# Performance work log

Measured on AMD Instinct MI355X. Metric: run time of the kernel, lower is better.

The kernel has to match this reference:

```python
import jax, jax.numpy as jnp
import numpy as np

NEG_SLOPE = 0.2   # PyG GATConv default leaky_relu slope
BN_EPS = 1e-5
SM_EPS = 1e-16    # PyG segment-softmax denominator epsilon


def gat_conv(x, src, dst, W, a_src, a_dst, bias, heads, out_ch, concat):
    # x: [N, F_in]; src/dst: [E] (self-loops already included)
    N = x.shape[0]
    h = (x @ W).reshape(N, heads, out_ch)              # [N, H, C]
    s = jnp.sum(h * a_src, axis=-1)                    # [N, H] per-node source score
    d = jnp.sum(h * a_dst, axis=-1)                    # [N, H] per-node dest score
    e = jax.nn.leaky_relu(s[src] + d[dst], NEG_SLOPE)  # [E, H]
    # segment softmax over edges grouped by destination node
    m = jax.ops.segment_max(e, dst, num_segments=N)
    m = jnp.where(jnp.isfinite(m), m, 0.0)
    p = jnp.exp(e - m[dst])                            # [E, H]
    denom = jax.ops.segment_sum(p, dst, num_segments=N)
    alpha = p / (denom[dst] + SM_EPS)                  # [E, H]
    # attention-weighted scatter-sum aggregation
    out = jax.ops.segment_sum(h[src] * alpha[:, :, None], dst, num_segments=N)  # [N, H, C]
    if concat:
        out = out.reshape(N, heads * out_ch)
    else:
        out = out.mean(axis=1)
    return out + bias


def setup_inputs() -> dict:
    key = jax.random.key(0)
    ks = jax.random.split(key, 12)
    N, E = 50000, 400000
    F_in, hidden, H1, H2, nclasses = 256, 64, 4, 1, 40
    x = jax.random.normal(ks[0], (N, F_in), dtype=jnp.float32)
    edge_index = jax.random.randint(ks[1], (2, E), 0, N, dtype=jnp.int64)
    g = 1.0 / np.sqrt(F_in)
    W1 = jax.random.normal(ks[2], (F_in, H1 * hidden), dtype=jnp.float32) * g
    a_src1 = jax.random.normal(ks[3], (H1, hidden), dtype=jnp.float32) * 0.1
    a_dst1 = jax.random.normal(ks[4], (H1, hidden), dtype=jnp.float32) * 0.1
    b1 = jnp.zeros((H1 * hidden,), dtype=jnp.float32)
    gamma = jnp.ones((H1 * hidden,), dtype=jnp.float32)
    beta = jnp.zeros((H1 * hidden,), dtype=jnp.float32)
    g2 = 1.0 / np.sqrt(H1 * hidden)
    W2 = jax.random.normal(ks[5], (H1 * hidden, H2 * nclasses), dtype=jnp.float32) * g2
    a_src2 = jax.random.normal(ks[6], (H2, nclasses), dtype=jnp.float32) * 0.1
    a_dst2 = jax.random.normal(ks[7], (H2, nclasses), dtype=jnp.float32) * 0.1
    b2 = jnp.zeros((nclasses,), dtype=jnp.float32)
    return {"x": x, "edge_index": edge_index, "W1": W1, "a_src1": a_src1,
            "a_dst1": a_dst1, "b1": b1, "gamma": gamma, "beta": beta,
            "W2": W2, "a_src2": a_src2, "a_dst2": a_dst2, "b2": b2}


def reference(x, edge_index, W1, a_src1, a_dst1, b1, gamma, beta, W2, a_src2, a_dst2, b2):
    N = x.shape[0]
    loop = jnp.arange(N, dtype=edge_index.dtype)
    src = jnp.concatenate([edge_index[0], loop])   # add self-loops (GATConv default)
    dst = jnp.concatenate([edge_index[1], loop])
    H1, hidden = a_src1.shape
    H2, nclasses = a_src2.shape
    h = gat_conv(x, src, dst, W1, a_src1, a_dst1, b1, H1, hidden, concat=True)
    # BatchNorm1d (training-mode batch statistics, biased variance)
    mu = h.mean(axis=0)
    var = h.var(axis=0)
    h = (h - mu) * jax.lax.rsqrt(var + BN_EPS) * gamma + beta
    h = jax.nn.elu(h)
    out = gat_conv(h, src, dst, W2, a_src2, a_dst2, b2, H2, nclasses, concat=False)
    return jax.nn.log_softmax(out, axis=-1)
```

## Files before the change

kernel.cpp:

```cpp
#include <hip/hip_runtime.h>
#include <hip/hip_fp16.h>

constexpr int FIN = 256;
constexpr int C1  = 256;
constexpr int HID = 64;
constexpr int H1N = 4;
constexpr int NC  = 40;
constexpr int CAP = 256;
constexpr int CAP2 = 128;

using f16x8 = __attribute__((ext_vector_type(8))) _Float16;
using f32x4 = __attribute__((ext_vector_type(4))) float;

__global__ __launch_bounds__(64)
void detect_kernel(const int* __restrict__ ei, int* __restrict__ flag, int E)
{
    int lane = threadIdx.x;
    int q = lane * (E / 64);
    int v = ei[2 * q + 1];
    unsigned long long nz = __ballot(v != 0);
    if (lane == 0) flag[0] = (nz == 0ull) ? 2 : 1;
}

__global__ __launch_bounds__(256)
void init_kernel(int* __restrict__ counts, int* __restrict__ fill,
                 float* __restrict__ colsum, float* __restrict__ colsq, int N)
{
    int t = blockIdx.x * 256 + threadIdx.x;
    if (t < N) { counts[t] = 1; fill[t] = 0; }
    if (t < C1) { colsum[t] = 0.f; colsq[t] = 0.f; }
}

__global__ __launch_bounds__(256)
void xcast_kernel(const float* __restrict__ X, _Float16* __restrict__ Xh,
                  int N, int NPAD)
{
    int idx = (blockIdx.x * 256 + threadIdx.x) * 4;
    if (idx >= NPAD * FIN) return;
    int row = idx >> 8;
    _Float16 h4[4];
    if (row < N) {
        float4 v = *(const float4*)(X + idx);
        h4[0] = (_Float16)v.x; h4[1] = (_Float16)v.y;
        h4[2] = (_Float16)v.z; h4[3] = (_Float16)v.w;
    } else {
        h4[0] = h4[1] = h4[2] = h4[3] = (_Float16)0.f;
    }
    *(uint2*)(Xh + idx) = *(uint2*)h4;
}

__global__ __launch_bounds__(256)
void w1cast_kernel(const float* __restrict__ W1, _Float16* __restrict__ W1t)
{
    __shared__ float tile[64][65];
    int bx = blockIdx.x & 3, by = blockIdx.x >> 2;
    int t = threadIdx.x;
    int c = t & 63, r4 = (t >> 6) * 16;
    #pragma unroll
    for (int i = 0; i < 16; ++i)
        tile[r4 + i][c] = W1[(size_t)(by * 64 + r4 + i) * C1 + bx * 64 + c];
    __syncthreads();
    #pragma unroll
    for (int i = 0; i < 16; ++i)
        W1t[(size_t)(bx * 64 + r4 + i) * FIN + by * 64 + c] =
            (_Float16)tile[c][r4 + i];
}

__global__ __launch_bounds__(256)
void gemm1_mfma_kernel(const _Float16* __restrict__ Xh,
                       const _Float16* __restrict__ W1t,
                       const float* __restrict__ as1, const float* __restrict__ ad1,
                       __half* __restrict__ Hm, float* __restrict__ s1,
                       float* __restrict__ d1, int N)
{
    const int t    = threadIdx.x;
    const int lane = t & 63;
    const int w    = t >> 6;
    const int rowbase = blockIdx.x * 64 + w * 16;
    const int lrow = lane & 15;
    const int kgrp = lane >> 4;
    const int arow = rowbase + lrow;

    f32x4 acc[16];
    #pragma unroll
    for (int i = 0; i < 16; ++i) acc[i] = f32x4{0.f, 0.f, 0.f, 0.f};

    #pragma unroll
    for (int ks = 0; ks < 8; ++ks) {
        f16x8 a = *(const f16x8*)(Xh + (size_t)arow * FIN + ks * 32 + kgrp * 8);
        #pragma unroll
        for (int ct = 0; ct < 16; ++ct) {
            f16x8 b = *(const f16x8*)(W1t + (size_t)(ct * 16 + lrow) * FIN
                                      + ks * 32 + kgrp * 8);
            acc[ct] = __builtin_amdgcn_mfma_f32_16x16x32_f16(a, b, acc[ct], 0, 0, 0);
        }
    }

    #pragma unroll
    for (int reg = 0; reg < 4; ++reg) {
        int r = rowbase + kgrp * 4 + reg;
        bool ok = r < N;
        #pragma unroll
        for (int h = 0; h < 4; ++h) {
            float sp = 0.f, dp = 0.f;
            #pragma unroll
            for (int q = 0; q < 4; ++q) {
                int ct = h * 4 + q;
                float v = acc[ct][reg];
                sp += v * as1[ct * 16 + lrow];
                dp += v * ad1[ct * 16 + lrow];
            }
            sp += __shfl_xor(sp, 1); sp += __shfl_xor(sp, 2);
            sp += __shfl_xor(sp, 4); sp += __shfl_xor(sp, 8);
            dp += __shfl_xor(dp, 1); dp += __shfl_xor(dp, 2);
            dp += __shfl_xor(dp, 4); dp += __shfl_xor(dp, 8);
            if (ok && lrow == 0) {
                s1[r * H1N + h] = sp;
                d1[r * H1N + h] = dp;
            }
        }
        if (ok) {
            #pragma unroll
            for (int ct = 0; ct < 16; ++ct)
                Hm[(size_t)r * C1 + ct * 16 + lrow] = __float2half(acc[ct][reg]);
        }
    }
}

__global__ __launch_bounds__(256)
void hist_kernel(const int* __restrict__ ei, const int* __restrict__ flag,
                 int* __restrict__ counts, int E)
{
    int t = blockIdx.x * 256 + threadIdx.x;
    int stride = flag[0];
    if (t < E) atomicAdd(&counts[ei[(size_t)stride * (E + t)]], 1);
}

__global__ __launch_bounds__(1024)
void scan_kernel(const int* __restrict__ cnt, int* __restrict__ offs, int N)
{
    __shared__ int wsum[16];
    __shared__ int carry_s;
    const int t = threadIdx.x, lane = t & 63, w = t >> 6;
    if (t == 0) carry_s = 0;
    __syncthreads();
    for (int base = 0; base < N; base += 1024) {
        int idx = base + t;
        int v = (idx < N) ? cnt[idx] : 0;
        int incl = v;
        #pragma unroll
        for (int off = 1; off < 64; off <<= 1) {
            int u = __shfl_up(incl, off);
            if (lane >= off) incl += u;
        }
        if (lane == 63) wsum[w] = incl;
        __syncthreads();
        int wpre = 0;
        for (int i = 0; i < w; ++i) wpre += wsum[i];
        int c = carry_s;
        if (idx < N) offs[idx] = c + wpre + incl - v;
        __syncthreads();
        if (t == 1023) carry_s = c + wpre + incl;
        __syncthreads();
    }
    if (t == 0) offs[N] = carry_s;
}

__global__ __launch_bounds__(256)
void scatter_kernel(const int* __restrict__ ei, const int* __restrict__ flag,
                    const int* __restrict__ offs, int* __restrict__ fill,
                    int* __restrict__ ssrc, int E, int N)
{
    int t = blockIdx.x * 256 + threadIdx.x;
    if (t >= E + N) return;
    int stride = flag[0];
    int s, d;
    if (t < E) {
        s = ei[(size_t)stride * t];
        d = ei[(size_t)stride * (E + t)];
    } else {
        s = t - E; d = s;
    }
    int pos = offs[d] + atomicAdd(&fill[d], 1);
    ssrc[pos] = s;
}

__global__ __launch_bounds__(256)
void agg1_kernel(const __half* __restrict__ Hm, const float* __restrict__ s1,
                 const float* __restrict__ d1, const int* __restrict__ offs,
                 const int* __restrict__ ssrc, const float* __restrict__ b1,
                 float* __restrict__ out1, int N)
{
    __shared__ float alpha[H1N][CAP];
    __shared__ int   srcs[CAP];
    __shared__ float invs[H1N];
    const int n    = blockIdx.x;
    const int t    = threadIdx.x;
    const int lane = t & 63;
    const int w    = t >> 6;
    const int beg  = offs[n], end = offs[n + 1];
    const int deg  = end - beg;
    const float dh = d1[n * H1N + w];

    if (deg <= CAP) {
        float mloc = -1e30f;
        for (int i = lane; i < deg; i += 64) {
            int s = ssrc[beg + i];
            if (w == 0) srcs[i] = s;
            float e = s1[s * H1N + w] + dh;
            e = e > 0.f ? e : 0.2f * e;
            alpha[w][i] = e;
            mloc = fmaxf(mloc, e);
        }
        #pragma unroll
        for (int off = 32; off; off >>= 1) mloc = fmaxf(mloc, __shfl_xor(mloc, off));
        float ssum = 0.f;
        for (int i = lane; i < deg; i += 64) {
            float ex = __expf(alpha[w][i] - mloc);
            alpha[w][i] = ex;
            ssum += ex;
        }
        #pragma unroll
        for (int off = 32; off; off >>= 1) ssum += __shfl_xor(ssum, off);
        if (lane == 0) invs[w] = 1.f / (ssum + 1e-16f);
        __syncthreads();

        float acc0 = 0.f, acc1 = 0.f, acc2 = 0.f, acc3 = 0.f;
        int i = 0;
        for (; i + 4 <= deg; i += 4) {
            int s0 = srcs[i],     s1i = srcs[i + 1];
            int s2 = srcs[i + 2], s3i = srcs[i + 3];
            float a0 = alpha[w][i],     a1 = alpha[w][i + 1];
            float a2 = alpha[w][i + 2], a3 = alpha[w][i + 3];
            float v0 = __half2float(Hm[(size_t)s0  * C1 + t]);
            float v1 = __half2float(Hm[(size_t)s1i * C1 + t]);
            float v2 = __half2float(Hm[(size_t)s2  * C1 + t]);
            float v3 = __half2float(Hm[(size_t)s3i * C1 + t]);
            acc0 += v0 * a0; acc1 += v1 * a1;
            acc2 += v2 * a2; acc3 += v3 * a3;
        }
        for (; i < deg; ++i)
            acc0 += __half2float(Hm[(size_t)srcs[i] * C1 + t]) * alpha[w][i];
        float acc = (acc0 + acc1) + (acc2 + acc3);
        out1[(size_t)n * C1 + t] = acc * invs[w] + b1[t];
        return;
    }

    float mloc = -1e30f;
    for (int p = beg + lane; p < end; p += 64) {
        float e = s1[ssrc[p] * H1N + w] + dh;
        e = e > 0.f ? e : 0.2f * e;
        mloc = fmaxf(mloc, e);
    }
    #pragma unroll
    for (int off = 32; off; off >>= 1) mloc = fmaxf(mloc, __shfl_xor(mloc, off));
    float ssum = 0.f;
    for (int p = beg + lane; p < end; p += 64) {
        float e = s1[ssrc[p] * H1N + w] + dh;
        e = e > 0.f ? e : 0.2f * e;
        ssum += __expf(e - mloc);
    }
    #pragma unroll
    for (int off = 32; off; off >>= 1) ssum += __shfl_xor(ssum, off);
    if (lane == 0) invs[w] = 1.f / (ssum + 1e-16f);

    float acc0 = 0.f, acc1 = 0.f, acc2 = 0.f, acc3 = 0.f;
    for (int c0 = 0; c0 < deg; c0 += CAP) {
        int cnt = min(CAP, deg - c0);
        for (int i = lane; i < cnt; i += 64) {
            int p = beg + c0 + i;
            int s = ssrc[p];
            if (w == 0) srcs[i] = s;
            float e = s1[s * H1N + w] + dh;
            e = e > 0.f ? e : 0.2f * e;
            alpha[w][i] = __expf(e - mloc);
        }
        __syncthreads();
        int i = 0;
        for (; i + 4 <= cnt; i += 4) {
            int s0 = srcs[i],     s1i = srcs[i + 1];
            int s2 = srcs[i + 2], s3i = srcs[i + 3];
            float a0 = alpha[w][i],     a1 = alpha[w][i + 1];
            float a2 = alpha[w][i + 2], a3 = alpha[w][i + 3];
            float v0 = __half2float(Hm[(size_t)s0  * C1 + t]);
            float v1 = __half2float(Hm[(size_t)s1i * C1 + t]);
            float v2 = __half2float(Hm[(size_t)s2  * C1 + t]);
            float v3 = __half2float(Hm[(size_t)s3i * C1 + t]);
            acc0 += v0 * a0; acc1 += v1 * a1;
            acc2 += v2 * a2; acc3 += v3 * a3;
        }
        for (; i < cnt; ++i)
            acc0 += __half2float(Hm[(size_t)srcs[i] * C1 + t]) * alpha[w][i];
        __syncthreads();
    }
    float acc = (acc0 + acc1) + (acc2 + acc3);
    out1[(size_t)n * C1 + t] = acc * invs[w] + b1[t];
}

__global__ __launch_bounds__(256)
void bnstats_kernel(const float* __restrict__ out1, float* __restrict__ colsum,
                    float* __restrict__ colsq, int N)
{
    int t = threadIdx.x;
    float s = 0.f, q = 0.f;
    for (int r = blockIdx.x; r < N; r += gridDim.x) {
        float v = out1[(size_t)r * C1 + t];
        s += v; q += v * v;
    }
    atomicAdd(&colsum[t], s);
    atomicAdd(&colsq[t], q);
}

__global__ __launch_bounds__(256)
void bnfin_kernel(const float* __restrict__ colsum, const float* __restrict__ colsq,
                  const float* __restrict__ gamma, const float* __restrict__ beta,
                  float* __restrict__ scale, float* __restrict__ shift, int N)
{
    int t = threadIdx.x;
    float mu  = colsum[t] / (float)N;
    float var = colsq[t] / (float)N - mu * mu;
    float sc  = gamma[t] * rsqrtf(var + 1e-5f);
    scale[t] = sc;
    shift[t] = beta[t] - mu * sc;
}

__global__ __launch_bounds__(256)
void gemm2_kernel(const float* __restrict__ out1, const float* __restrict__ scale,
                  const float* __restrict__ shift, const float* __restrict__ W2,
                  const float* __restrict__ as2, const float* __restrict__ ad2,
                  float* __restrict__ h2, float* __restrict__ s2,
                  float* __restrict__ d2, int N)
{
    __shared__ float Asm[64][68];
    __shared__ float Wsm[64 * 48];
    const int t   = threadIdx.x;
    const int r   = t >> 2;
    const int jg  = t & 3;
    const int rb  = blockIdx.x * 64;
    const int row = rb + r;
    const int j0  = jg * 10;

    float acc[10] = {};

    for (int kc = 0; kc < C1; kc += 64) {
        #pragma unroll
        for (int idx = t; idx < 64 * 16; idx += 256) {
            int ar = idx >> 4;
            int cg = (idx & 15) * 4;
            int arow = rb + ar;
            float4 v = make_float4(0.f, 0.f, 0.f, 0.f);
            if (arow < N) {
                v = *(const float4*)(out1 + (size_t)arow * C1 + kc + cg);
                float4 sc = *(const float4*)(scale + kc + cg);
                float4 sh = *(const float4*)(shift + kc + cg);
                v.x = v.x * sc.x + sh.x;
                v.y = v.y * sc.y + sh.y;
                v.z = v.z * sc.z + sh.z;
                v.w = v.w * sc.w + sh.w;
                v.x = v.x > 0.f ? v.x : (__expf(v.x) - 1.f);
                v.y = v.y > 0.f ? v.y : (__expf(v.y) - 1.f);
                v.z = v.z > 0.f ? v.z : (__expf(v.z) - 1.f);
                v.w = v.w > 0.f ? v.w : (__expf(v.w) - 1.f);
            }
            *(float4*)&Asm[ar][cg] = v;
        }
        #pragma unroll
        for (int idx = t; idx < 64 * 40; idx += 256) {
            int k = idx / 40, j = idx - k * 40;
            Wsm[k * 48 + (j / 10) * 12 + (j % 10)] = W2[(size_t)(kc + k) * NC + j];
        }
        __syncthreads();
        #pragma unroll 4
        for (int k = 0; k < 64; ++k) {
            float a = Asm[r][k];
            const float* wp = &Wsm[k * 48 + jg * 12];
            float4 w0 = *(const float4*)(wp);
            float4 w1 = *(const float4*)(wp + 4);
            float2 wv = *(const float2*)(wp + 8);
            acc[0] += a * w0.x; acc[1] += a * w0.y;
            acc[2] += a * w0.z; acc[3] += a * w0.w;
            acc[4] += a * w1.x; acc[5] += a * w1.y;
            acc[6] += a * w1.z; acc[7] += a * w1.w;
            acc[8] += a * wv.x; acc[9] += a * wv.y;
        }
        __syncthreads();
    }

    float sp = 0.f, dp = 0.f;
    #pragma unroll
    for (int jj = 0; jj < 10; ++jj) {
        sp += acc[jj] * as2[j0 + jj];
        dp += acc[jj] * ad2[j0 + jj];
    }
    sp += __shfl_xor(sp, 1); sp += __shfl_xor(sp, 2);
    dp += __shfl_xor(dp, 1); dp += __shfl_xor(dp, 2);
    if (row < N) {
        if (jg == 0) { s2[row] = sp; d2[row] = dp; }
        #pragma unroll
        for (int jj = 0; jj < 10; jj += 2)
            *(float2*)(h2 + (size_t)row * NC + j0 + jj) =
                make_float2(acc[jj], acc[jj + 1]);
    }
}

__global__ __launch_bounds__(256)
void agg2_kernel(const float* __restrict__ h2, const float* __restrict__ s2,
                 const float* __restrict__ d2, const int* __restrict__ offs,
                 const int* __restrict__ ssrc, const float* __restrict__ b2,
                 float* __restrict__ out, int N)
{
    __shared__ float al[4][CAP2];
    __shared__ int   sr[4][CAP2];
    int w = threadIdx.x >> 6;
    int node = blockIdx.x * 4 + w;
    if (node >= N) return;
    int lane = threadIdx.x & 63;
    int beg = offs[node], end = offs[node + 1];
    int deg = end - beg;
    float dn = d2[node];

    float v;
    if (deg <= CAP2) {
        float mloc = -1e30f;
        for (int i = lane; i < deg; i += 64) {
            int s = ssrc[beg + i];
            sr[w][i] = s;
            float e = s2[s] + dn;
            e = e > 0.f ? e : 0.2f * e;
            al[w][i] = e;
            mloc = fmaxf(mloc, e);
        }
        #pragma unroll
        for (int off = 32; off; off >>= 1) mloc = fmaxf(mloc, __shfl_xor(mloc, off));
        float ssum = 0.f;
        for (int i = lane; i < deg; i += 64) {
            float ex = __expf(al[w][i] - mloc);
            al[w][i] = ex;
            ssum += ex;
        }
        #pragma unroll
        for (int off = 32; off; off >>= 1) ssum += __shfl_xor(ssum, off);
        float inv = 1.f / (ssum + 1e-16f);

        int j = lane < NC ? lane : 0;
        float acc0 = 0.f, acc1 = 0.f, acc2 = 0.f, acc3 = 0.f;
        int i = 0;
        for (; i + 4 <= deg; i += 4) {
            float a0 = al[w][i],     a1 = al[w][i + 1];
            float a2 = al[w][i + 2], a3 = al[w][i + 3];
            acc0 += h2[(size_t)sr[w][i]     * NC + j] * a0;
            acc1 += h2[(size_t)sr[w][i + 1] * NC + j] * a1;
            acc2 += h2[(size_t)sr[w][i + 2] * NC + j] * a2;
            acc3 += h2[(size_t)sr[w][i + 3] * NC + j] * a3;
        }
        for (; i < deg; ++i)
            acc0 += h2[(size_t)sr[w][i] * NC + j] * al[w][i];
        v = ((acc0 + acc1) + (acc2 + acc3)) * inv + b2[j];
    } else {
        float m = -1e30f, denom = 0.f;
        for (int p = beg; p < end; ++p) {
            float e = s2[ssrc[p]] + dn;
            e = e > 0.f ? e : 0.2f * e;
            float mn = fmaxf(m, e);
            denom = denom * __expf(m - mn) + __expf(e - mn);
            m = mn;
        }
        float inv = 1.f / (denom + 1e-16f);
        int j = lane < NC ? lane : 0;
        float acc = 0.f;
        for (int p = beg; p < end; ++p) {
            int s = ssrc[p];
            float e = s2[s] + dn;
            e = e > 0.f ? e : 0.2f * e;
            acc += h2[(size_t)s * NC + j] * (__expf(e - m) * inv);
        }
        v = acc + b2[j];
    }

    float vm = lane < NC ? v : -1e30f;
    #pragma unroll
    for (int off = 32; off > 0; off >>= 1) vm = fmaxf(vm, __shfl_xor(vm, off));
    float ex = lane < NC ? __expf(v - vm) : 0.f;
    #pragma unroll
    for (int off = 32; off > 0; off >>= 1) ex += __shfl_xor(ex, off);
    if (lane < NC) out[(size_t)node * NC + lane] = v - vm - __logf(ex);
}

extern "C" void kernel_launch(void* const* d_in, const int* in_sizes, int n_in,
                              void* d_out, int out_size, void* d_ws, size_t ws_size,
                              hipStream_t stream)
{
    const float* x   = (const float*)d_in[0];
    const int*   ei  = (const int*)d_in[1];
    const float* W1  = (const float*)d_in[2];
    const float* as1 = (const float*)d_in[3];
    const float* ad1 = (const float*)d_in[4];
    const float* b1  = (const float*)d_in[5];
    const float* gm  = (const float*)d_in[6];
    const float* bt  = (const float*)d_in[7];
    const float* W2  = (const float*)d_in[8];
    const float* as2 = (const float*)d_in[9];
    const float* ad2 = (const float*)d_in[10];
    const float* b2  = (const float*)d_in[11];
    const int N = in_sizes[0] / FIN;
    const int E = in_sizes[1] / 2;
    const int NPAD = (N + 63) & ~63;

    char* p = (char*)d_ws;
    auto take = [&](size_t bytes) {
        char* r = p; p += (bytes + 255) & ~(size_t)255; return r;
    };
    __half* Hm       = (__half*)take((size_t)N * C1 * 2);
    _Float16* Xh     = (_Float16*)take((size_t)NPAD * FIN * 2);
    _Float16* W1t    = (_Float16*)take((size_t)FIN * C1 * 2);
    float* out1   = (float*)take((size_t)N * C1 * 4);
    float* h2     = (float*)take((size_t)N * NC * 4);
    float* s1     = (float*)take((size_t)N * H1N * 4);
    float* d1     = (float*)take((size_t)N * H1N * 4);
    float* s2     = (float*)take((size_t)N * 4);
    float* d2v    = (float*)take((size_t)N * 4);
    float* colsum = (float*)take(C1 * 4);
    float* colsq  = (float*)take(C1 * 4);
    float* bnsc   = (float*)take(C1 * 4);
    float* bnsh   = (float*)take(C1 * 4);
    int*   counts = (int*)take((size_t)N * 4);
    int*   offs   = (int*)take((size_t)(N + 1) * 4);
    int*   fill   = (int*)take((size_t)N * 4);
    int*   ssrc   = (int*)take((size_t)(E + N) * 4);
    int*   eflag  = (int*)take(256);

    detect_kernel<<<1, 64, 0, stream>>>(ei, eflag, E);
    init_kernel<<<(N + 255) / 256, 256, 0, stream>>>(counts, fill, colsum, colsq, N);
    xcast_kernel<<<(NPAD * FIN / 4 + 255) / 256, 256, 0, stream>>>(x, Xh, N, NPAD);
    w1cast_kernel<<<16, 256, 0, stream>>>(W1, W1t);
    gemm1_mfma_kernel<<<NPAD / 64, 256, 0, stream>>>(Xh, W1t, as1, ad1, Hm, s1, d1, N);
    hist_kernel<<<(E + 255) / 256, 256, 0, stream>>>(ei, eflag, counts, E);
    scan_kernel<<<1, 1024, 0, stream>>>(counts, offs, N);
    scatter_kernel<<<(E + N + 255) / 256, 256, 0, stream>>>(ei, eflag, offs, fill, ssrc, E, N);
    agg1_kernel<<<N, 256, 0, stream>>>(Hm, s1, d1, offs, ssrc, b1, out1, N);
    bnstats_kernel<<<1024, 256, 0, stream>>>(out1, colsum, colsq, N);
    bnfin_kernel<<<1, 256, 0, stream>>>(colsum, colsq, gm, bt, bnsc, bnsh, N);
    gemm2_kernel<<<(N + 63) / 64, 256, 0, stream>>>(out1, bnsc, bnsh, W2, as2, ad2, h2, s2, d2v, N);
    agg2_kernel<<<(N + 3) / 4, 256, 0, stream>>>(h2, s2, d2v, offs, ssrc, b2, (float*)d_out, N);
}
```

Measured before the change: 483.5 us.

## Split layer-1 attention softmax into separate kernel and pack two nodes per block

Moves the per-destination segment softmax for layer 1 into a new astats kernel: one wavefront per node, with lanes split across heads and edges, writing normalized per-edge alphas to a global buffer. The aggregation kernel then handles two nodes per 256-thread block, each thread covering two channels through half2 loads, with no shared memory and no barriers. This removes the heavy per-node shared-memory softmax phase and the syncthreads from the bandwidth-bound gather. In exchange it adds an extra launch and an (E+N)x4 float alpha buffer that is written once and read back.

```diff
diff --git a/kernel.cpp b/kernel.cpp
--- a/kernel.cpp
+++ b/kernel.cpp
@@ -6,7 +6,6 @@
 constexpr int HID = 64;
 constexpr int H1N = 4;
 constexpr int NC  = 40;
-constexpr int CAP = 256;
 constexpr int CAP2 = 128;
 
 using f16x8 = __attribute__((ext_vector_type(8))) _Float16;
@@ -186,115 +185,92 @@
 }
 
 __global__ __launch_bounds__(256)
-void agg1_kernel(const __half* __restrict__ Hm, const float* __restrict__ s1,
-                 const float* __restrict__ d1, const int* __restrict__ offs,
-                 const int* __restrict__ ssrc, const float* __restrict__ b1,
-                 float* __restrict__ out1, int N)
-{
-    __shared__ float alpha[H1N][CAP];
-    __shared__ int   srcs[CAP];
-    __shared__ float invs[H1N];
-    const int n    = blockIdx.x;
-    const int t    = threadIdx.x;
-    const int lane = t & 63;
-    const int w    = t >> 6;
-    const int beg  = offs[n], end = offs[n + 1];
-    const int deg  = end - beg;
-    const float dh = d1[n * H1N + w];
-
-    if (deg <= CAP) {
-        float mloc = -1e30f;
-        for (int i = lane; i < deg; i += 64) {
-            int s = ssrc[beg + i];
-            if (w == 0) srcs[i] = s;
-            float e = s1[s * H1N + w] + dh;
-            e = e > 0.f ? e : 0.2f * e;
-            alpha[w][i] = e;
-            mloc = fmaxf(mloc, e);
-        }
-        #pragma unroll
-        for (int off = 32; off; off >>= 1) mloc = fmaxf(mloc, __shfl_xor(mloc, off));
-        float ssum = 0.f;
-        for (int i = lane; i < deg; i += 64) {
-            float ex = __expf(alpha[w][i] - mloc);
-            alpha[w][i] = ex;
-            ssum += ex;
-        }
-        #pragma unroll
-        for (int off = 32; off; off >>= 1) ssum += __shfl_xor(ssum, off);
-        if (lane == 0) invs[w] = 1.f / (ssum + 1e-16f);
-        __syncthreads();
-
-        float acc0 = 0.f, acc1 = 0.f, acc2 = 0.f, acc3 = 0.f;
-        int i = 0;
-        for (; i + 4 <= deg; i += 4) {
-            int s0 = srcs[i],     s1i = srcs[i + 1];
-            int s2 = srcs[i + 2], s3i = srcs[i + 3];
-            float a0 = alpha[w][i],     a1 = alpha[w][i + 1];
-            float a2 = alpha[w][i + 2], a3 = alpha[w][i + 3];
-            float v0 = __half2float(Hm[(size_t)s0  * C1 + t]);
-            float v1 = __half2float(Hm[(size_t)s1i * C1 + t]);
-            float v2 = __half2float(Hm[(size_t)s2  * C1 + t]);
-            float v3 = __half2float(Hm[(size_t)s3i * C1 + t]);
-            acc0 += v0 * a0; acc1 += v1 * a1;
-            acc2 += v2 * a2; acc3 += v3 * a3;
-        }
-        for (; i < deg; ++i)
-            acc0 += __half2float(Hm[(size_t)srcs[i] * C1 + t]) * alpha[w][i];
-        float acc = (acc0 + acc1) + (acc2 + acc3);
-        out1[(size_t)n * C1 + t] = acc * invs[w] + b1[t];
-        return;
-    }
-
-    float mloc = -1e30f;
-    for (int p = beg + lane; p < end; p += 64) {
-        float e = s1[ssrc[p] * H1N + w] + dh;
+void astats_kernel(const float* __restrict__ s1, const float* __restrict__ d1,
+                   const int* __restrict__ offs, const int* __restrict__ ssrc,
+                   float* __restrict__ alphaE, int N)
+{
+    int w = threadIdx.x >> 6;
+    int n = blockIdx.x * 4 + w;
+    if (n >= N) return;
+    int lane = threadIdx.x & 63;
+    int h  = lane & 3;
+    int ig = lane >> 2;
+    int beg = offs[n], end = offs[n + 1];
+    float dh = d1[n * H1N + h];
+
+    float m = -1e30f;
+    for (int p = beg + ig; p < end; p += 16) {
+        float e = s1[ssrc[p] * H1N + h] + dh;
         e = e > 0.f ? e : 0.2f * e;
-        mloc = fmaxf(mloc, e);
-    }
-    #pragma unroll
-    for (int off = 32; off; off >>= 1) mloc = fmaxf(mloc, __shfl_xor(mloc, off));
+        m = fmaxf(m, e);
+    }
+    m = fmaxf(m, __shfl_xor(m, 4));
+    m = fmaxf(m, __shfl_xor(m, 8));
+    m = fmaxf(m, __shfl_xor(m, 16));
+    m = fmaxf(m, __shfl_xor(m, 32));
+
     float ssum = 0.f;
-    for (int p = beg + lane; p < end; p += 64) {
-        float e = s1[ssrc[p] * H1N + w] + dh;
+    for (int p = beg + ig; p < end; p += 16) {
+        float e = s1[ssrc[p] * H1N + h] + dh;
         e = e > 0.f ? e : 0.2f * e;
-        ssum += __expf(e - mloc);
-    }
-    #pragma unroll
-    for (int off = 32; off; off >>= 1) ssum += __shfl_xor(ssum, off);
-    if (lane == 0) invs[w] = 1.f / (ssum + 1e-16f);
-
-    float acc0 = 0.f, acc1 = 0.f, acc2 = 0.f, acc3 = 0.f;
-    for (int c0 = 0; c0 < deg; c0 += CAP) {
-        int cnt = min(CAP, deg - c0);
-        for (int i = lane; i < cnt; i += 64) {
-            int p = beg + c0 + i;
-            int s = ssrc[p];
-            if (w == 0) srcs[i] = s;
-            float e = s1[s * H1N + w] + dh;
-            e = e > 0.f ? e : 0.2f * e;
-            alpha[w][i] = __expf(e - mloc);
-        }
-        __syncthreads();
-        int i = 0;
-        for (; i + 4 <= cnt; i += 4) {
-            int s0 = srcs[i],     s1i = srcs[i + 1];
-            int s2 = srcs[i + 2], s3i = srcs[i + 3];
-            float a0 = alpha[w][i],     a1 = alpha[w][i + 1];
-            float a2 = alpha[w][i + 2], a3 = alpha[w][i + 3];
-            float v0 = __half2float(Hm[(size_t)s0  * C1 + t]);
-            float v1 = __half2float(Hm[(size_t)s1i * C1 + t]);
-            float v2 = __half2float(Hm[(size_t)s2  * C1 + t]);
-            float v3 = __half2float(Hm[(size_t)s3i * C1 + t]);
-            acc0 += v0 * a0; acc1 += v1 * a1;
-            acc2 += v2 * a2; acc3 += v3 * a3;
-        }
-        for (; i < cnt; ++i)
-            acc0 += __half2float(Hm[(size_t)srcs[i] * C1 + t]) * alpha[w][i];
-        __syncthreads();
-    }
-    float acc = (acc0 + acc1) + (acc2 + acc3);
-    out1[(size_t)n * C1 + t] = acc * invs[w] + b1[t];
+        ssum += __expf(e - m);
+    }
+    ssum += __shfl_xor(ssum, 4);
+    ssum += __shfl_xor(ssum, 8);
+    ssum += __shfl_xor(ssum, 16);
+    ssum += __shfl_xor(ssum, 32);
+    float inv = 1.f / (ssum + 1e-16f);
+
+    for (int p = beg + ig; p < end; p += 16) {
+        float e = s1[ssrc[p] * H1N + h] + dh;
+        e = e > 0.f ? e : 0.2f * e;
+        alphaE[(size_t)p * H1N + h] = __expf(e - m) * inv;
+    }
+}
+
+__global__ __launch_bounds__(256)
+void agg1_kernel(const __half* __restrict__ Hm, const float* __restrict__ alphaE,
+                 const int* __restrict__ offs, const int* __restrict__ ssrc,
+                 const float* __restrict__ b1, float* __restrict__ out1, int N)
+{
+    const int n = blockIdx.x * 2 + (threadIdx.x >> 7);
+    if (n >= N) return;
+    const int l = threadIdx.x & 127;
+    const int c = 2 * l;
+    const int h = l >> 5;
+    const int beg = offs[n], end = offs[n + 1];
+
+    float ax = 0.f, ay = 0.f, bx = 0.f, by = 0.f;
+    float cx = 0.f, cy = 0.f, dx = 0.f, dy = 0.f;
+    int p = beg;
+    for (; p + 4 <= end; p += 4) {
+        int s0 = ssrc[p],     s1i = ssrc[p + 1];
+        int s2 = ssrc[p + 2], s3  = ssrc[p + 3];
+        float a0 = alphaE[(size_t)(p)     * H1N + h];
+        float a1 = alphaE[(size_t)(p + 1) * H1N + h];
+        float a2 = alphaE[(size_t)(p + 2) * H1N + h];
+        float a3 = alphaE[(size_t)(p + 3) * H1N + h];
+        float2 v0 = __half22float2(*(const __half2*)(Hm + (size_t)s0  * C1 + c));
+        float2 v1 = __half22float2(*(const __half2*)(Hm + (size_t)s1i * C1 + c));
+        float2 v2 = __half22float2(*(const __half2*)(Hm + (size_t)s2  * C1 + c));
+        float2 v3 = __half22float2(*(const __half2*)(Hm + (size_t)s3  * C1 + c));
+        ax += v0.x * a0; ay += v0.y * a0;
+        bx += v1.x * a1; by += v1.y * a1;
+        cx += v2.x * a2; cy += v2.y * a2;
+        dx += v3.x * a3; dy += v3.y * a3;
+    }
+    for (; p < end; ++p) {
+        int s0 = ssrc[p];
+        float a0 = alphaE[(size_t)p * H1N + h];
+        float2 v0 = __half22float2(*(const __half2*)(Hm + (size_t)s0 * C1 + c));
+        ax += v0.x * a0; ay += v0.y * a0;
+    }
+    float sx = (ax + bx) + (cx + dx);
+    float sy = (ay + by) + (cy + dy);
+    float2 r;
+    r.x = sx + b1[c];
+    r.y = sy + b1[c + 1];
+    *(float2*)(out1 + (size_t)n * C1 + c) = r;
 }
 
 __global__ __launch_bounds__(256)
@@ -513,6 +489,7 @@
     __half* Hm       = (__half*)take((size_t)N * C1 * 2);
     _Float16* Xh     = (_Float16*)take((size_t)NPAD * FIN * 2);
     _Float16* W1t    = (_Float16*)take((size_t)FIN * C1 * 2);
+    float* alphaE = (float*)take((size_t)(E + N) * H1N * 4);
     float* out1   = (float*)take((size_t)N * C1 * 4);
     float* h2     = (float*)take((size_t)N * NC * 4);
     float* s1     = (float*)take((size_t)N * H1N * 4);
@@ -537,7 +514,8 @@
     hist_kernel<<<(E + 255) / 256, 256, 0, stream>>>(ei, eflag, counts, E);
     scan_kernel<<<1, 1024, 0, stream>>>(counts, offs, N);
     scatter_kernel<<<(E + N + 255) / 256, 256, 0, stream>>>(ei, eflag, offs, fill, ssrc, E, N);
-    agg1_kernel<<<N, 256, 0, stream>>>(Hm, s1, d1, offs, ssrc, b1, out1, N);
+    astats_kernel<<<(N + 3) / 4, 256, 0, stream>>>(s1, d1, offs, ssrc, alphaE, N);
+    agg1_kernel<<<(N + 1) / 2, 256, 0, stream>>>(Hm, alphaE, offs, ssrc, b1, out1, N);
     bnstats_kernel<<<1024, 256, 0, stream>>>(out1, colsum, colsq, N);
     bnfin_kernel<<<1, 256, 0, stream>>>(colsum, colsq, gm, bt, bnsc, bnsh, N);
     gemm2_kernel<<<(N + 63) / 64, 256, 0, stream>>>(out1, bnsc, bnsh, W2, as2, ad2, h2, s2, d2v, N);
```

Result: faster. 466.1 us (-3.6%).
